# Kernel tuning notes

Hardware: AMD Instinct MI355X
Metric: run time of the kernel (lower is better)

The kernel has to match this reference:

```python
import jax, jax.numpy as jnp
import numpy as np

B, H, S, DK = 2, 16, 2048, 64
NEG = -1e9

def setup_inputs() -> dict:
    key = jax.random.key(0)
    kq, kk, kv, km, kmask = jax.random.split(key, 5)
    Q = jax.random.normal(kq, (B, H, S, DK), dtype=jnp.float32)
    K = jax.random.normal(kk, (B, H, S, DK), dtype=jnp.float32)
    V = jax.random.normal(kv, (B, H, S, DK), dtype=jnp.float32)
    matrix = jax.random.uniform(km, (B, H, S, S), dtype=jnp.float32)
    attn_mask = jax.random.randint(kmask, (B, H, S, S), 0, 2).astype(jnp.bool_)
    return {"Q": Q, "K": K, "V": V, "attn_mask": attn_mask, "matrix": matrix}

def reference(Q, K, V, attn_mask, matrix):
    # scores = (Q K^T / sqrt(d_k)) * matrix, masked_fill, softmax, @ V (dropout p=0)
    scores = jnp.einsum('bhqd,bhkd->bhqk', Q, K) / jnp.sqrt(jnp.float32(DK))
    scores = scores * matrix
    scores = jnp.where(attn_mask, jnp.float32(NEG), scores)
    attn = jax.nn.softmax(scores, axis=-1)
    context = jnp.einsum('bhqk,bhkd->bhqd', attn, V)
    return context
```

## Files before the change

kernel.cpp:

```cpp
#include <hip/hip_runtime.h>
#include <hip/hip_fp16.h>

#define S_DIM 2048
#define D_K   64
#define BQ    64
#define BK    64
#define KSTR  72
#define NEGV  -1e9f

typedef _Float16 f16;
typedef f16  f16x2 __attribute__((ext_vector_type(2)));
typedef f16  f16x4 __attribute__((ext_vector_type(4)));
typedef f16  f16x8 __attribute__((ext_vector_type(8)));
typedef float f32x4 __attribute__((ext_vector_type(4)));

__global__ void mask_probe(const unsigned int* __restrict__ mw, int* __restrict__ flag) {
    int t = threadIdx.x;
    unsigned int isFloat = 0u, gt1 = 0u;
#pragma unroll
    for (int i = 0; i < 16; ++i) {
        unsigned int v = mw[t * 16 + i];
        isFloat |= (v == 0x3f800000u) ? 1u : 0u;
        gt1     |= (v > 1u) ? 1u : 0u;
    }
    if (isFloat) atomicOr(flag, 2);
    else if (gt1) atomicOr(flag, 1);
}

__global__ __launch_bounds__(256, 4)
void attn_kernel(const float* __restrict__ Qg, const float* __restrict__ Kg,
                 const float* __restrict__ Vg, const void* __restrict__ maskp,
                 const float* __restrict__ Mg, float* __restrict__ Og,
                 const int* __restrict__ flagp)
{
    const int bh  = blockIdx.y;
    const int q0  = blockIdx.x * BQ;
    const int tid = threadIdx.x;
    const int wv  = tid >> 6;
    const int ln  = tid & 63;
    const int n16 = ln & 15;
    const int qd  = ln >> 4;

    const int fl   = *flagp;
    const int mfmt = (fl & 2) ? 2 : (fl & 1);

    const size_t bhQ = (size_t)bh * S_DIM * D_K;
    const float* Qp = Qg + bhQ;
    const float* Kp = Kg + bhQ;
    const float* Vp = Vg + bhQ;
    const size_t bhS = (size_t)bh * S_DIM * S_DIM;
    const float*         Mp = Mg + bhS;
    const unsigned char* mB = (const unsigned char*)maskp + bhS;
    const int*           mI = (const int*)maskp + bhS;
    const float*         mF = (const float*)maskp + bhS;

    __shared__ f16 Ksh[BK][KSTR];
    __shared__ f16 Vsh[D_K][KSTR];
    __shared__ f16 Psh[4][16][KSTR];

    f16x8 qa[2];
    {
        const float* qp = Qp + (size_t)(q0 + wv * 16 + n16) * D_K + qd * 8;
#pragma unroll
        for (int kc = 0; kc < 2; ++kc) {
            float4 x0 = *(const float4*)(qp + kc * 32);
            float4 x1 = *(const float4*)(qp + kc * 32 + 4);
            f16x8 a;
            a[0]=(f16)(x0.x*0.125f); a[1]=(f16)(x0.y*0.125f);
            a[2]=(f16)(x0.z*0.125f); a[3]=(f16)(x0.w*0.125f);
            a[4]=(f16)(x1.x*0.125f); a[5]=(f16)(x1.y*0.125f);
            a[6]=(f16)(x1.z*0.125f); a[7]=(f16)(x1.w*0.125f);
            qa[kc] = a;
        }
    }

    float m_i[4], l_i[4];
    f32x4 oa[4];
#pragma unroll
    for (int r = 0; r < 4; ++r) { m_i[r] = -3.0e38f; l_i[r] = 0.f; }
#pragma unroll
    for (int nc = 0; nc < 4; ++nc) oa[nc] = (f32x4){0.f, 0.f, 0.f, 0.f};

    const int qrow0 = q0 + wv * 16 + qd * 4;

    for (int kb = 0; kb < S_DIM / BK; ++kb) {
        const int k0 = kb * BK;
        __syncthreads();

#pragma unroll
        for (int i = 0; i < 4; ++i) {
            int fidx = tid + i * 256;
            int key  = fidx >> 4;
            int dk4  = (fidx & 15) << 2;
            float4 kv = *(const float4*)(Kp + (size_t)(k0 + key) * D_K + dk4);
            f16x4 h; h[0]=(f16)kv.x; h[1]=(f16)kv.y; h[2]=(f16)kv.z; h[3]=(f16)kv.w;
            *(f16x4*)&Ksh[key][dk4] = h;
        }
#pragma unroll
        for (int i = 0; i < 2; ++i) {
            int fidx = tid + i * 256;
            int kp2  = fidx >> 4;
            int dk4  = (fidx & 15) << 2;
            const float* vp = Vp + (size_t)(k0 + kp2 * 2) * D_K + dk4;
            float4 v0 = *(const float4*)(vp);
            float4 v1 = *(const float4*)(vp + D_K);
            float v0a[4] = {v0.x, v0.y, v0.z, v0.w};
            float v1a[4] = {v1.x, v1.y, v1.z, v1.w};
#pragma unroll
            for (int c = 0; c < 4; ++c) {
                f16x2 h; h[0] = (f16)v0a[c]; h[1] = (f16)v1a[c];
                *(f16x2*)&Vsh[dk4 + c][kp2 * 2] = h;
            }
        }
        __syncthreads();

        float mt[4][4];
        int mbits = 0;
        {
            const size_t base = (size_t)qrow0 * S_DIM + k0 + n16;
#pragma unroll
            for (int r = 0; r < 4; ++r)
#pragma unroll
                for (int cc = 0; cc < 4; ++cc)
                    mt[r][cc] = __builtin_nontemporal_load(Mp + base + (size_t)r * S_DIM + cc * 16);
            if (mfmt == 1) {
#pragma unroll
                for (int r = 0; r < 4; ++r)
#pragma unroll
                    for (int cc = 0; cc < 4; ++cc)
                        if (__builtin_nontemporal_load(mB + base + (size_t)r * S_DIM + cc * 16))
                            mbits |= 1 << (r * 4 + cc);
            } else if (mfmt == 0) {
#pragma unroll
                for (int r = 0; r < 4; ++r)
#pragma unroll
                    for (int cc = 0; cc < 4; ++cc)
                        if (__builtin_nontemporal_load(mI + base + (size_t)r * S_DIM + cc * 16))
                            mbits |= 1 << (r * 4 + cc);
            } else {
#pragma unroll
                for (int r = 0; r < 4; ++r)
#pragma unroll
                    for (int cc = 0; cc < 4; ++cc)
                        if (__builtin_nontemporal_load(mF + base + (size_t)r * S_DIM + cc * 16) != 0.f)
                            mbits |= 1 << (r * 4 + cc);
            }
        }

        f32x4 sc[4];
#pragma unroll
        for (int cc = 0; cc < 4; ++cc) {
            f32x4 acc = (f32x4){0.f, 0.f, 0.f, 0.f};
#pragma unroll
            for (int kc = 0; kc < 2; ++kc) {
                f16x8 b = *(const f16x8*)&Ksh[cc * 16 + n16][kc * 32 + qd * 8];
                acc = __builtin_amdgcn_mfma_f32_16x16x32_f16(qa[kc], b, acc, 0, 0, 0);
            }
            sc[cc] = acc;
        }

#pragma unroll
        for (int cc = 0; cc < 4; ++cc)
#pragma unroll
            for (int r = 0; r < 4; ++r) {
                float s = sc[cc][r] * mt[r][cc];
                sc[cc][r] = ((mbits >> (r * 4 + cc)) & 1) ? NEGV : s;
            }

        float alpha[4];
#pragma unroll
        for (int r = 0; r < 4; ++r) {
            float rm = fmaxf(fmaxf(sc[0][r], sc[1][r]), fmaxf(sc[2][r], sc[3][r]));
#pragma unroll
            for (int off = 1; off < 16; off <<= 1)
                rm = fmaxf(rm, __shfl_xor(rm, off, 64));
            float mn = fmaxf(m_i[r], rm);
            alpha[r] = __expf(m_i[r] - mn);
            m_i[r] = mn;
        }
        float rs[4] = {0.f, 0.f, 0.f, 0.f};
#pragma unroll
        for (int cc = 0; cc < 4; ++cc)
#pragma unroll
            for (int r = 0; r < 4; ++r) {
                float p = __expf(sc[cc][r] - m_i[r]);
                sc[cc][r] = p;
                rs[r] += p;
            }
#pragma unroll
        for (int r = 0; r < 4; ++r) {
#pragma unroll
            for (int off = 1; off < 16; off <<= 1)
                rs[r] += __shfl_xor(rs[r], off, 64);
            l_i[r] = l_i[r] * alpha[r] + rs[r];
        }

#pragma unroll
        for (int cc = 0; cc < 4; ++cc)
#pragma unroll
            for (int r = 0; r < 4; ++r)
                Psh[wv][qd * 4 + r][cc * 16 + n16] = (f16)sc[cc][r];

#pragma unroll
        for (int nc = 0; nc < 4; ++nc)
#pragma unroll
            for (int r = 0; r < 4; ++r)
                oa[nc][r] *= alpha[r];

#pragma unroll
        for (int kc = 0; kc < 2; ++kc) {
            f16x8 a = *(const f16x8*)&Psh[wv][n16][kc * 32 + qd * 8];
#pragma unroll
            for (int nc = 0; nc < 4; ++nc) {
                f16x8 b = *(const f16x8*)&Vsh[nc * 16 + n16][kc * 32 + qd * 8];
                oa[nc] = __builtin_amdgcn_mfma_f32_16x16x32_f16(a, b, oa[nc], 0, 0, 0);
            }
        }
    }

#pragma unroll
    for (int r = 0; r < 4; ++r) {
        float inv = 1.f / l_i[r];
#pragma unroll
        for (int nc = 0; nc < 4; ++nc) {
            size_t off = ((size_t)bh * S_DIM + (qrow0 + r)) * D_K + nc * 16 + n16;
            __builtin_nontemporal_store(oa[nc][r] * inv, Og + off);
        }
    }
}

extern "C" void kernel_launch(void* const* d_in, const int* in_sizes, int n_in,
                              void* d_out, int out_size, void* d_ws, size_t ws_size,
                              hipStream_t stream) {
    const float* Q      = (const float*)d_in[0];
    const float* K      = (const float*)d_in[1];
    const float* V      = (const float*)d_in[2];
    const void*  mask   = d_in[3];
    const float* matrix = (const float*)d_in[4];
    float* out = (float*)d_out;
    int* flag = (int*)d_ws;

    hipMemsetAsync(flag, 0, sizeof(int), stream);
    mask_probe<<<1, 256, 0, stream>>>((const unsigned int*)mask, flag);

    dim3 grid(S_DIM / BQ, 2 * 16);
    attn_kernel<<<grid, 256, 0, stream>>>(Q, K, V, mask, matrix, out, flag);
}
```

Baseline: 1.065 ms.

## Use exp2 softmax with MFMA row sums, lazy rescale, and swizzled V tile

Folds log2(e) into the Q scale so the softmax uses exp2f. The row sum now comes from an extra MFMA against a ones vector instead of shuffle reductions, and the row-max reduction is done in packed fp16. Rescaling of the accumulators is skipped when no row max grows anywhere in the wavefront. The V shared tile uses an XOR swizzle in place of padding to avoid bank conflicts. These changes cut shuffle and exp work per tile, but the fp16 max and the -3e4 clamp could change precision slightly.

After: 1.064 ms. Within noise of the previous version (-0.1%).

```diff
diff --git a/kernel.cpp b/kernel.cpp
--- a/kernel.cpp
+++ b/kernel.cpp
@@ -7,6 +7,7 @@
 #define BK    64
 #define KSTR  72
 #define NEGV  -1e9f
+#define LOG2E 1.44269504088896f
 
 typedef _Float16 f16;
 typedef f16  f16x2 __attribute__((ext_vector_type(2)));
@@ -55,9 +56,10 @@
     const float*         mF = (const float*)maskp + bhS;
 
     __shared__ f16 Ksh[BK][KSTR];
-    __shared__ f16 Vsh[D_K][KSTR];
+    __shared__ f16 Vsh[D_K][D_K];
     __shared__ f16 Psh[4][16][KSTR];
 
+    const float QSC = 0.125f * LOG2E;
     f16x8 qa[2];
     {
         const float* qp = Qp + (size_t)(q0 + wv * 16 + n16) * D_K + qd * 8;
@@ -66,20 +68,25 @@
             float4 x0 = *(const float4*)(qp + kc * 32);
             float4 x1 = *(const float4*)(qp + kc * 32 + 4);
             f16x8 a;
-            a[0]=(f16)(x0.x*0.125f); a[1]=(f16)(x0.y*0.125f);
-            a[2]=(f16)(x0.z*0.125f); a[3]=(f16)(x0.w*0.125f);
-            a[4]=(f16)(x1.x*0.125f); a[5]=(f16)(x1.y*0.125f);
-            a[6]=(f16)(x1.z*0.125f); a[7]=(f16)(x1.w*0.125f);
+            a[0]=(f16)(x0.x*QSC); a[1]=(f16)(x0.y*QSC);
+            a[2]=(f16)(x0.z*QSC); a[3]=(f16)(x0.w*QSC);
+            a[4]=(f16)(x1.x*QSC); a[5]=(f16)(x1.y*QSC);
+            a[6]=(f16)(x1.z*QSC); a[7]=(f16)(x1.w*QSC);
             qa[kc] = a;
         }
     }
 
-    float m_i[4], l_i[4];
-    f32x4 oa[4];
-#pragma unroll
-    for (int r = 0; r < 4; ++r) { m_i[r] = -3.0e38f; l_i[r] = 0.f; }
+    f16x8 vone;
+#pragma unroll
+    for (int j = 0; j < 8; ++j) vone[j] = (f16)1.0f;
+
+    float m_i[4];
+    f32x4 oa[4], ol;
+#pragma unroll
+    for (int r = 0; r < 4; ++r) m_i[r] = -3.0e38f;
 #pragma unroll
     for (int nc = 0; nc < 4; ++nc) oa[nc] = (f32x4){0.f, 0.f, 0.f, 0.f};
+    ol = (f32x4){0.f, 0.f, 0.f, 0.f};
 
     const int qrow0 = q0 + wv * 16 + qd * 4;
 
@@ -100,16 +107,17 @@
         for (int i = 0; i < 2; ++i) {
             int fidx = tid + i * 256;
             int kp2  = fidx >> 4;
-            int dk4  = (fidx & 15) << 2;
-            const float* vp = Vp + (size_t)(k0 + kp2 * 2) * D_K + dk4;
+            int u    = fidx & 15;
+            const float* vp = Vp + (size_t)(k0 + kp2 * 2) * D_K + u * 4;
             float4 v0 = *(const float4*)(vp);
             float4 v1 = *(const float4*)(vp + D_K);
             float v0a[4] = {v0.x, v0.y, v0.z, v0.w};
             float v1a[4] = {v1.x, v1.y, v1.z, v1.w};
+            int pp = kp2 ^ ((u & 7) << 2);
 #pragma unroll
             for (int c = 0; c < 4; ++c) {
                 f16x2 h; h[0] = (f16)v0a[c]; h[1] = (f16)v1a[c];
-                *(f16x2*)&Vsh[dk4 + c][kp2 * 2] = h;
+                *(f16x2*)&Vsh[u * 4 + c][pp * 2] = h;
             }
         }
         __syncthreads();
@@ -167,52 +175,57 @@
                 sc[cc][r] = ((mbits >> (r * 4 + cc)) & 1) ? NEGV : s;
             }
 
-        float alpha[4];
+        float rm[4];
 #pragma unroll
         for (int r = 0; r < 4; ++r) {
-            float rm = fmaxf(fmaxf(sc[0][r], sc[1][r]), fmaxf(sc[2][r], sc[3][r]));
-#pragma unroll
-            for (int off = 1; off < 16; off <<= 1)
-                rm = fmaxf(rm, __shfl_xor(rm, off, 64));
-            float mn = fmaxf(m_i[r], rm);
-            alpha[r] = __expf(m_i[r] - mn);
-            m_i[r] = mn;
-        }
-        float rs[4] = {0.f, 0.f, 0.f, 0.f};
+            rm[r] = fmaxf(fmaxf(sc[0][r], sc[1][r]), fmaxf(sc[2][r], sc[3][r]));
+            rm[r] = fmaxf(rm[r], -3.0e4f);
+        }
+        {
+            union HU { f16x2 h; int u; };
+            HU a, b, t;
+            a.h[0] = (f16)rm[0]; a.h[1] = (f16)rm[1];
+            b.h[0] = (f16)rm[2]; b.h[1] = (f16)rm[3];
+#pragma unroll
+            for (int off = 1; off < 16; off <<= 1) {
+                t.u = __shfl_xor(a.u, off, 64);
+                a.h = __builtin_elementwise_max(a.h, t.h);
+                t.u = __shfl_xor(b.u, off, 64);
+                b.h = __builtin_elementwise_max(b.h, t.h);
+            }
+            rm[0] = (float)a.h[0]; rm[1] = (float)a.h[1];
+            rm[2] = (float)b.h[0]; rm[3] = (float)b.h[1];
+        }
+
+        int grow = (rm[0] > m_i[0]) | (rm[1] > m_i[1]) |
+                   (rm[2] > m_i[2]) | (rm[3] > m_i[3]);
+        if (__any(grow)) {
+#pragma unroll
+            for (int r = 0; r < 4; ++r) {
+                float mn = fmaxf(m_i[r], rm[r]);
+                float al = exp2f(m_i[r] - mn);
+                m_i[r] = mn;
+#pragma unroll
+                for (int nc = 0; nc < 4; ++nc) oa[nc][r] *= al;
+                ol[r] *= al;
+            }
+        }
+
 #pragma unroll
         for (int cc = 0; cc < 4; ++cc)
 #pragma unroll
-            for (int r = 0; r < 4; ++r) {
-                float p = __expf(sc[cc][r] - m_i[r]);
-                sc[cc][r] = p;
-                rs[r] += p;
-            }
-#pragma unroll
-        for (int r = 0; r < 4; ++r) {
-#pragma unroll
-            for (int off = 1; off < 16; off <<= 1)
-                rs[r] += __shfl_xor(rs[r], off, 64);
-            l_i[r] = l_i[r] * alpha[r] + rs[r];
-        }
-
-#pragma unroll
-        for (int cc = 0; cc < 4; ++cc)
-#pragma unroll
             for (int r = 0; r < 4; ++r)
-                Psh[wv][qd * 4 + r][cc * 16 + n16] = (f16)sc[cc][r];
-
-#pragma unroll
-        for (int nc = 0; nc < 4; ++nc)
-#pragma unroll
-            for (int r = 0; r < 4; ++r)
-                oa[nc][r] *= alpha[r];
+                Psh[wv][qd * 4 + r][cc * 16 + n16] = (f16)exp2f(sc[cc][r] - m_i[r]);
 
 #pragma unroll
         for (int kc = 0; kc < 2; ++kc) {
             f16x8 a = *(const f16x8*)&Psh[wv][n16][kc * 32 + qd * 8];
+            ol = __builtin_amdgcn_mfma_f32_16x16x32_f16(a, vone, ol, 0, 0, 0);
 #pragma unroll
             for (int nc = 0; nc < 4; ++nc) {
-                f16x8 b = *(const f16x8*)&Vsh[nc * 16 + n16][kc * 32 + qd * 8];
+                int sdw = (nc * 4 + (n16 >> 2)) & 7;
+                int pb  = (16 * kc + 4 * qd) ^ (sdw << 2);
+                f16x8 b = *(const f16x8*)&Vsh[nc * 16 + n16][pb * 2];
                 oa[nc] = __builtin_amdgcn_mfma_f32_16x16x32_f16(a, b, oa[nc], 0, 0, 0);
             }
         }
@@ -220,7 +233,7 @@
 
 #pragma unroll
     for (int r = 0; r < 4; ++r) {
-        float inv = 1.f / l_i[r];
+        float inv = 1.f / ol[r];
 #pragma unroll
         for (int nc = 0; nc < 4; ++nc) {
             size_t off = ((size_t)bh * S_DIM + (qrow0 + r)) * D_K + nc * 16 + n16;
```
